# Kernel optimization log

Measured on AMD Instinct MI355X. Metric: run time of the kernel, lower is better.

Reference implementation:

```python
import jax, jax.numpy as jnp
import numpy as np

B, C, D, H, W = 16, 8, 511, 16, 16
NHEADS = 16
DIM = C * H * W          # 2048 hidden size
SEQ = D + 1              # 512 tokens incl. cls
HEAD_DIM = DIM // NHEADS # 128


def setup_inputs() -> dict:
    key = jax.random.key(0)
    ks = jax.random.split(key, 8)
    s = 0.02  # weight init scale
    return {
        "x": jax.random.normal(ks[0], (B, C, D, H, W), jnp.float32),
        "pos_embedding": jax.random.normal(ks[1], (1, SEQ, DIM), jnp.float32),
        "cls": jax.random.normal(ks[2], (1, 1, DIM), jnp.float32),
        "qkv_w": jax.random.normal(ks[3], (DIM, 3 * DIM), jnp.float32) * s,
        "qkv_b": jnp.zeros((3 * DIM,), jnp.float32),
        "proj_w": jax.random.normal(ks[4], (DIM, DIM), jnp.float32) * s,
        "proj_b": jnp.zeros((DIM,), jnp.float32),
    }


def reference(x, pos_embedding, cls, qkv_w, qkv_b, proj_w, proj_b):
    b = x.shape[0]
    # rearrange 'b c d h w -> b d (c h w)'
    tok = jnp.transpose(x, (0, 2, 1, 3, 4)).reshape(b, D, DIM)
    tok = jnp.concatenate([jnp.broadcast_to(cls, (b, 1, DIM)), tok], axis=1)
    tok = tok + pos_embedding  # (b, SEQ, DIM)
    # qkv projection (dropout probs are 0 -> identity)
    qkv = tok @ qkv_w + qkv_b  # (b, SEQ, 3*DIM)
    qkv = qkv.reshape(b, SEQ, 3, NHEADS, HEAD_DIM).transpose(2, 0, 3, 1, 4)
    q, k, v = qkv[0], qkv[1], qkv[2]  # each (b, nH, SEQ, hd)
    scale = HEAD_DIM ** -0.5
    score = jax.nn.softmax(jnp.einsum('bhqd,bhkd->bhqk', q, k) * scale, axis=-1)
    out = jnp.einsum('bhqk,bhkd->bhqd', score, v)
    out = out.transpose(0, 2, 1, 3).reshape(b, SEQ, DIM)
    out = out @ proj_w + proj_b
    return out[:, 0]  # cls token, (b, DIM)
```

## Files before the change

kernel.cpp:

```cpp
#include <hip/hip_runtime.h>


#define BB   16
#define CC   8
#define DD   511
#define DIM  2048
#define SEQ  512
#define NH   16
#define HD   128
#define W3   6144
#define SCALE 0.08838834764831845f

#define Q_OFF   0
#define AO_OFF  2048
#define G_OFF   34816
#define SC_OFF  34832
#define ZERO_N  165904
#define R_OFF   165904
#define RB_OFF  198672
#define U_OFF   231440

typedef __attribute__((ext_vector_type(8))) short short8;
typedef __attribute__((ext_vector_type(4))) float floatx4;

static __device__ inline short bf_hi(float f) {
  return (short)(__float_as_uint(f) >> 16);
}
static __device__ inline float bf_hif(float f) {
  return __uint_as_float(__float_as_uint(f) & 0xffff0000u);
}

__global__ __launch_bounds__(256) void k1_q(
    const float* __restrict__ pos, const float* __restrict__ cls,
    const float* __restrict__ qkv_w, const float* __restrict__ qkv_b,
    float* __restrict__ ws) {
  int n  = blockIdx.x * 256 + threadIdx.x;
  int d0 = blockIdx.y * 32;
  float acc = (blockIdx.y == 0) ? qkv_b[n] : 0.f;
#pragma unroll 8
  for (int d = d0; d < d0 + 32; ++d) {
    float t0 = cls[d] + pos[d];
    acc += t0 * qkv_w[(size_t)d * W3 + n];
  }
  atomicAdd(&ws[Q_OFF + n], acc);
}

__global__ __launch_bounds__(128) void k2_r(
    const float* __restrict__ qkv_w, const float* __restrict__ pos,
    const float* __restrict__ cls, float* __restrict__ ws) {
  __shared__ float qs[HD];
  int h = blockIdx.y;
  int d = blockIdx.x * 128 + threadIdx.x;
  if (threadIdx.x < HD) qs[threadIdx.x] = ws[Q_OFF + h * HD + threadIdx.x];
  __syncthreads();
  const float4* w4 = reinterpret_cast<const float4*>(
      qkv_w + (size_t)d * W3 + DIM + h * HD);
  float acc = 0.f;
#pragma unroll 8
  for (int e4 = 0; e4 < 32; ++e4) {
    float4 w = w4[e4];
    acc += qs[e4*4+0]*w.x + qs[e4*4+1]*w.y + qs[e4*4+2]*w.z + qs[e4*4+3]*w.w;
  }
  float r = acc * SCALE;
  int i = h * DIM + d;
  ws[R_OFF + i] = r;
  short* rb = (short*)(ws + RB_OFF);
  rb[i] = bf_hi(r);
  rb[NH * DIM + i] = bf_hi(r - bf_hif(r));
  float g = (cls[d] + pos[d]) * r;
  for (int m = 1; m < 64; m <<= 1) g += __shfl_xor(g, m, 64);
  if ((threadIdx.x & 63) == 0) atomicAdd(&ws[G_OFF + h], g);
}

__global__ __launch_bounds__(64) void k3_scores_mfma(
    const float* __restrict__ x, const float* __restrict__ pos,
    float* __restrict__ ws) {
  int jt = blockIdx.x, b = blockIdx.y, ks = blockIdx.z;
  int l  = threadIdx.x;
  int m  = l & 15;
  int kg = l >> 4;
  int jrow = 1 + jt * 16 + m;
  int jc = jrow < SEQ ? jrow : (SEQ - 1);
  const size_t xrow = (size_t)b * CC * DD * 256 + (size_t)(jc - 1) * 256;
  const short* rh = (const short*)(ws + RB_OFF);
  const short* rl = rh + NH * DIM;
  floatx4 acc = {0.f, 0.f, 0.f, 0.f};
#pragma unroll 2
  for (int kk = ks * 16; kk < ks * 16 + 16; ++kk) {
    int d0 = kk * 32 + kg * 8;
    int c = d0 >> 8, doff = d0 & 255;
    const float4* xp = reinterpret_cast<const float4*>(
        x + xrow + (size_t)c * DD * 256 + doff);
    const float4* pp = reinterpret_cast<const float4*>(
        pos + (size_t)jc * DIM + d0);
    float4 xa = xp[0], xb = xp[1];
    float4 pa = pp[0], pb = pp[1];
    float f[8] = {xa.x + pa.x, xa.y + pa.y, xa.z + pa.z, xa.w + pa.w,
                  xb.x + pb.x, xb.y + pb.y, xb.z + pb.z, xb.w + pb.w};
    short8 ahi, alo;
#pragma unroll
    for (int i = 0; i < 8; ++i) {
      ahi[i] = bf_hi(f[i]);
      alo[i] = bf_hi(f[i] - bf_hif(f[i]));
    }
    short8 bhi = *reinterpret_cast<const short8*>(rh + m * DIM + d0);
    short8 blo = *reinterpret_cast<const short8*>(rl + m * DIM + d0);
    acc = __builtin_amdgcn_mfma_f32_16x16x32_bf16(ahi, bhi, acc, 0, 0, 0);
    acc = __builtin_amdgcn_mfma_f32_16x16x32_bf16(ahi, blo, acc, 0, 0, 0);
    acc = __builtin_amdgcn_mfma_f32_16x16x32_bf16(alo, bhi, acc, 0, 0, 0);
  }
  int h = m;
#pragma unroll
  for (int reg = 0; reg < 4; ++reg) {
    int row = kg * 4 + reg;
    int j = 1 + jt * 16 + row;
    if (j < SEQ)
      atomicAdd(&ws[SC_OFF + (size_t)(b * NH + h) * SEQ + j], acc[reg]);
  }
}

__global__ __launch_bounds__(256) void k4_softmax(float* __restrict__ ws) {
  int h = blockIdx.x, b = blockIdx.y, t = threadIdx.x;
  float* sc = ws + SC_OFF + (size_t)(b * NH + h) * SEQ;
  __shared__ float red[256];
  float s0 = (t == 0) ? ws[G_OFF + h] : sc[t];
  float s1 = sc[t + 256];
  red[t] = fmaxf(s0, s1);
  __syncthreads();
  for (int s = 128; s > 0; s >>= 1) { if (t < s) red[t] = fmaxf(red[t], red[t + s]); __syncthreads(); }
  float m = red[0];
  __syncthreads();
  float e0 = __expf(s0 - m), e1 = __expf(s1 - m);
  red[t] = e0 + e1;
  __syncthreads();
  for (int s = 128; s > 0; s >>= 1) { if (t < s) red[t] += red[t + s]; __syncthreads(); }
  float inv = 1.f / red[0];
  sc[t] = e0 * inv;
  sc[t + 256] = e1 * inv;
}

#define PSTR 520
__global__ __launch_bounds__(256) void k5_pv_mfma(
    const float* __restrict__ x, const float* __restrict__ pos,
    const float* __restrict__ cls, float* __restrict__ ws) {
  int dt = blockIdx.x, b = blockIdx.y, t = threadIdx.x;
  __shared__ short phl[NH * PSTR];
  __shared__ short pll[NH * PSTR];
  const float* pb = ws + SC_OFF + (size_t)b * NH * SEQ;
  for (int i = t; i < NH * SEQ; i += 256) {
    int h = i >> 9, j = i & 511;
    float v = pb[h * SEQ + j];
    phl[h * PSTR + j] = bf_hi(v);
    pll[h * PSTR + j] = bf_hi(v - bf_hif(v));
  }
  __syncthreads();
  int w = t >> 6, l = t & 63;
  int m16 = l & 15, kq = l >> 4;
  int dcol = dt * 64 + w * 16 + m16;
  int c = dcol >> 8, doff = dcol & 255;
  const float* xcol = x + (size_t)b * CC * DD * 256 + (size_t)c * DD * 256 + doff;
  const float* pcol = pos + dcol;
  float clsv0 = cls[dcol];
  const short8* pph = reinterpret_cast<const short8*>(&phl[m16 * PSTR]);
  const short8* ppl = reinterpret_cast<const short8*>(&pll[m16 * PSTR]);
  floatx4 acc = {0.f, 0.f, 0.f, 0.f};
  for (int kk = 0; kk < 16; ++kk) {
    int jb = kk * 32 + kq * 8;
    const float* xp = xcol + ((size_t)jb - 1) * 256;
    const float* xp_safe = (jb == 0) ? xcol : xp;
    float f[8];
    float x0 = xp_safe[0];
    f[0] = ((jb == 0) ? clsv0 : x0) + pcol[(size_t)jb * DIM];
#pragma unroll
    for (int e = 1; e < 8; ++e)
      f[e] = xp[(size_t)e * 256] + pcol[(size_t)(jb + e) * DIM];
    short8 thi, tlo;
#pragma unroll
    for (int i = 0; i < 8; ++i) {
      thi[i] = bf_hi(f[i]);
      tlo[i] = bf_hi(f[i] - bf_hif(f[i]));
    }
    short8 phi = pph[kk * 4 + kq];
    short8 plo = ppl[kk * 4 + kq];
    acc = __builtin_amdgcn_mfma_f32_16x16x32_bf16(phi, thi, acc, 0, 0, 0);
    acc = __builtin_amdgcn_mfma_f32_16x16x32_bf16(phi, tlo, acc, 0, 0, 0);
    acc = __builtin_amdgcn_mfma_f32_16x16x32_bf16(plo, thi, acc, 0, 0, 0);
  }
  float* ub = ws + U_OFF + (size_t)b * NH * DIM + dcol;
#pragma unroll
  for (int reg = 0; reg < 4; ++reg) {
    int h = kq * 4 + reg;
    ub[(size_t)h * DIM] = acc[reg];
  }
}

__global__ __launch_bounds__(256) void k6_ao(
    const float* __restrict__ qkv_w, const float* __restrict__ qkv_b,
    float* __restrict__ ws) {
  int nt = blockIdx.x, dc = blockIdx.y, t = threadIdx.x;
  int m = nt * 256 + t;
  int h0 = nt * 2;
  int d0 = dc * 32;
  __shared__ float us[2][32][20];
  for (int i = t; i < 2 * 32 * BB; i += 256) {
    int dd = i & 31, b = (i >> 5) & 15, hh = i >> 9;
    us[hh][dd][b] = ws[U_OFF + (size_t)(b * NH + h0 + hh) * DIM + d0 + dd];
  }
  __syncthreads();
  int hl = t >> 7;
  float acc[BB];
#pragma unroll
  for (int b = 0; b < BB; ++b) acc[b] = 0.f;
  const float* wcol = qkv_w + (size_t)d0 * W3 + 2 * DIM + m;
#pragma unroll 4
  for (int dd = 0; dd < 32; ++dd) {
    float w = wcol[(size_t)dd * W3];
    const float4* u4 = reinterpret_cast<const float4*>(&us[hl][dd][0]);
    float4 u0 = u4[0], u1 = u4[1], u2 = u4[2], u3 = u4[3];
    acc[0]  += u0.x * w; acc[1]  += u0.y * w; acc[2]  += u0.z * w; acc[3]  += u0.w * w;
    acc[4]  += u1.x * w; acc[5]  += u1.y * w; acc[6]  += u1.z * w; acc[7]  += u1.w * w;
    acc[8]  += u2.x * w; acc[9]  += u2.y * w; acc[10] += u2.z * w; acc[11] += u2.w * w;
    acc[12] += u3.x * w; acc[13] += u3.y * w; acc[14] += u3.z * w; acc[15] += u3.w * w;
  }
  float bias = (dc == 0) ? qkv_b[2 * DIM + m] : 0.f;
#pragma unroll
  for (int b = 0; b < BB; ++b)
    atomicAdd(&ws[AO_OFF + b * DIM + m], acc[b] + bias);
}

__global__ __launch_bounds__(256) void k7_out(
    const float* __restrict__ proj_w, const float* __restrict__ proj_b,
    const float* __restrict__ ws, float* __restrict__ out) {
  int nt = blockIdx.x, mc = blockIdx.y, t = threadIdx.x;
  int n = nt * 256 + t;
  int m0 = mc * 32;
  __shared__ float as[32][20];
  for (int i = t; i < 32 * BB; i += 256) {
    int mm = i & 31, b = i >> 5;
    as[mm][b] = ws[AO_OFF + b * DIM + m0 + mm];
  }
  __syncthreads();
  float acc[BB];
#pragma unroll
  for (int b = 0; b < BB; ++b) acc[b] = 0.f;
  const float* wcol = proj_w + (size_t)m0 * DIM + n;
#pragma unroll 4
  for (int mm = 0; mm < 32; ++mm) {
    float w = wcol[(size_t)mm * DIM];
    const float4* a4 = reinterpret_cast<const float4*>(&as[mm][0]);
    float4 a0 = a4[0], a1 = a4[1], a2 = a4[2], a3 = a4[3];
    acc[0]  += a0.x * w; acc[1]  += a0.y * w; acc[2]  += a0.z * w; acc[3]  += a0.w * w;
    acc[4]  += a1.x * w; acc[5]  += a1.y * w; acc[6]  += a1.z * w; acc[7]  += a1.w * w;
    acc[8]  += a2.x * w; acc[9]  += a2.y * w; acc[10] += a2.z * w; acc[11] += a2.w * w;
    acc[12] += a3.x * w; acc[13] += a3.y * w; acc[14] += a3.z * w; acc[15] += a3.w * w;
  }
  float bias = (mc == 0) ? proj_b[n] : 0.f;
#pragma unroll
  for (int b = 0; b < BB; ++b)
    atomicAdd(&out[b * DIM + n], acc[b] + bias);
}

extern "C" void kernel_launch(void* const* d_in, const int* in_sizes, int n_in,
                              void* d_out, int out_size, void* d_ws, size_t ws_size,
                              hipStream_t stream) {
  const float* x      = (const float*)d_in[0];
  const float* pos    = (const float*)d_in[1];
  const float* cls    = (const float*)d_in[2];
  const float* qkv_w  = (const float*)d_in[3];
  const float* qkv_b  = (const float*)d_in[4];
  const float* proj_w = (const float*)d_in[5];
  const float* proj_b = (const float*)d_in[6];
  float* ws  = (float*)d_ws;
  float* out = (float*)d_out;

  hipMemsetAsync(ws, 0, (size_t)ZERO_N * sizeof(float), stream);
  hipMemsetAsync(out, 0, (size_t)out_size * sizeof(float), stream);

  k1_q          <<<dim3(8, 64),     256, 0, stream>>>(pos, cls, qkv_w, qkv_b, ws);
  k2_r          <<<dim3(16, 16),    128, 0, stream>>>(qkv_w, pos, cls, ws);
  k3_scores_mfma<<<dim3(32, 16, 4),  64, 0, stream>>>(x, pos, ws);
  k4_softmax    <<<dim3(16, 16),    256, 0, stream>>>(ws);
  k5_pv_mfma    <<<dim3(32, 16),    256, 0, stream>>>(x, pos, cls, ws);
  k6_ao         <<<dim3(8, 64),     256, 0, stream>>>(qkv_w, qkv_b, ws);
  k7_out        <<<dim3(8, 64),     256, 0, stream>>>(proj_w, proj_b, ws, out);
}
```

Measured before the change: 222.1 us.

## Fuse all seven stages into one cooperative persistent kernel with grid syncs

```diff
diff --git a/kernel.cpp b/kernel.cpp
--- a/kernel.cpp
+++ b/kernel.cpp
@@ -1,4 +1,7 @@
 #include <hip/hip_runtime.h>
+#include <hip/hip_cooperative_groups.h>
+
+namespace cg = cooperative_groups;
 
 
 #define BB   16
@@ -10,15 +13,18 @@
 #define HD   128
 #define W3   6144
 #define SCALE 0.08838834764831845f
+#define GRID 512
 
 #define Q_OFF   0
-#define AO_OFF  2048
-#define G_OFF   34816
+#define G_OFF   2048
+#define AO_OFF  2064
 #define SC_OFF  34832
 #define ZERO_N  165904
 #define R_OFF   165904
 #define RB_OFF  198672
 #define U_OFF   231440
+
+#define PSTR 520
 
 typedef __attribute__((ext_vector_type(8))) short short8;
 typedef __attribute__((ext_vector_type(4))) float floatx4;
@@ -30,234 +36,252 @@
   return __uint_as_float(__float_as_uint(f) & 0xffff0000u);
 }
 
-__global__ __launch_bounds__(256) void k1_q(
-    const float* __restrict__ pos, const float* __restrict__ cls,
-    const float* __restrict__ qkv_w, const float* __restrict__ qkv_b,
-    float* __restrict__ ws) {
-  int n  = blockIdx.x * 256 + threadIdx.x;
-  int d0 = blockIdx.y * 32;
-  float acc = (blockIdx.y == 0) ? qkv_b[n] : 0.f;
+struct PVShared { short phl[NH * PSTR]; short pll[NH * PSTR]; };
+union Shared {
+  PVShared pv;
+  float qs[HD];
+  float red[256];
+  float us[2][32][20];
+  float as[32][20];
+};
+
+__global__ __launch_bounds__(256, 2) void vit_fused(
+    const float* __restrict__ x, const float* __restrict__ pos,
+    const float* __restrict__ cls, const float* __restrict__ qkv_w,
+    const float* __restrict__ qkv_b, const float* __restrict__ proj_w,
+    const float* __restrict__ proj_b, float* __restrict__ ws,
+    float* __restrict__ out) {
+  cg::grid_group grid = cg::this_grid();
+  __shared__ Shared sh;
+  const int blk = blockIdx.x;
+  const int t   = threadIdx.x;
+
+  for (int i = blk * 256 + t; i < ZERO_N; i += GRID * 256) ws[i] = 0.f;
+  for (int i = blk * 256 + t; i < BB * DIM; i += GRID * 256) out[i] = 0.f;
+  grid.sync();
+
+  {
+    int nt = blk & 7, dch = blk >> 3;
+    int n = nt * 256 + t, d0 = dch * 32;
+    float acc = (dch == 0) ? qkv_b[n] : 0.f;
 #pragma unroll 8
-  for (int d = d0; d < d0 + 32; ++d) {
-    float t0 = cls[d] + pos[d];
-    acc += t0 * qkv_w[(size_t)d * W3 + n];
-  }
-  atomicAdd(&ws[Q_OFF + n], acc);
-}
-
-__global__ __launch_bounds__(128) void k2_r(
-    const float* __restrict__ qkv_w, const float* __restrict__ pos,
-    const float* __restrict__ cls, float* __restrict__ ws) {
-  __shared__ float qs[HD];
-  int h = blockIdx.y;
-  int d = blockIdx.x * 128 + threadIdx.x;
-  if (threadIdx.x < HD) qs[threadIdx.x] = ws[Q_OFF + h * HD + threadIdx.x];
-  __syncthreads();
-  const float4* w4 = reinterpret_cast<const float4*>(
-      qkv_w + (size_t)d * W3 + DIM + h * HD);
-  float acc = 0.f;
+    for (int d = d0; d < d0 + 32; ++d) {
+      float t0 = cls[d] + pos[d];
+      acc += t0 * qkv_w[(size_t)d * W3 + n];
+    }
+    atomicAdd(&ws[Q_OFF + n], acc);
+  }
+  grid.sync();
+
+  if (blk < 128) {
+    int h = blk >> 3, dt = blk & 7;
+    int d = dt * 256 + t;
+    if (t < HD) sh.qs[t] = ws[Q_OFF + h * HD + t];
+    __syncthreads();
+    const float4* w4 = reinterpret_cast<const float4*>(
+        qkv_w + (size_t)d * W3 + DIM + h * HD);
+    float acc = 0.f;
 #pragma unroll 8
-  for (int e4 = 0; e4 < 32; ++e4) {
-    float4 w = w4[e4];
-    acc += qs[e4*4+0]*w.x + qs[e4*4+1]*w.y + qs[e4*4+2]*w.z + qs[e4*4+3]*w.w;
-  }
-  float r = acc * SCALE;
-  int i = h * DIM + d;
-  ws[R_OFF + i] = r;
-  short* rb = (short*)(ws + RB_OFF);
-  rb[i] = bf_hi(r);
-  rb[NH * DIM + i] = bf_hi(r - bf_hif(r));
-  float g = (cls[d] + pos[d]) * r;
-  for (int m = 1; m < 64; m <<= 1) g += __shfl_xor(g, m, 64);
-  if ((threadIdx.x & 63) == 0) atomicAdd(&ws[G_OFF + h], g);
-}
-
-__global__ __launch_bounds__(64) void k3_scores_mfma(
-    const float* __restrict__ x, const float* __restrict__ pos,
-    float* __restrict__ ws) {
-  int jt = blockIdx.x, b = blockIdx.y, ks = blockIdx.z;
-  int l  = threadIdx.x;
-  int m  = l & 15;
-  int kg = l >> 4;
-  int jrow = 1 + jt * 16 + m;
-  int jc = jrow < SEQ ? jrow : (SEQ - 1);
-  const size_t xrow = (size_t)b * CC * DD * 256 + (size_t)(jc - 1) * 256;
-  const short* rh = (const short*)(ws + RB_OFF);
-  const short* rl = rh + NH * DIM;
-  floatx4 acc = {0.f, 0.f, 0.f, 0.f};
+    for (int e4 = 0; e4 < 32; ++e4) {
+      float4 w = w4[e4];
+      acc += sh.qs[e4*4+0]*w.x + sh.qs[e4*4+1]*w.y
+           + sh.qs[e4*4+2]*w.z + sh.qs[e4*4+3]*w.w;
+    }
+    float r = acc * SCALE;
+    int i = h * DIM + d;
+    ws[R_OFF + i] = r;
+    short* rb = (short*)(ws + RB_OFF);
+    rb[i] = bf_hi(r);
+    rb[NH * DIM + i] = bf_hi(r - bf_hif(r));
+    float g = (cls[d] + pos[d]) * r;
+    for (int m = 1; m < 64; m <<= 1) g += __shfl_xor(g, m, 64);
+    if ((t & 63) == 0) atomicAdd(&ws[G_OFF + h], g);
+  }
+  grid.sync();
+
+  {
+    int jt2 = blk & 7, b = (blk >> 3) & 15, ks = blk >> 7;
+    int w = t >> 6, l = t & 63;
+    int jt = jt2 * 4 + w;
+    int m16 = l & 15, kg = l >> 4;
+    int jrow = 1 + jt * 16 + m16;
+    int jc = jrow < SEQ ? jrow : (SEQ - 1);
+    const size_t xrow = (size_t)b * CC * DD * 256 + (size_t)(jc - 1) * 256;
+    const short* rh = (const short*)(ws + RB_OFF);
+    const short* rl = rh + NH * DIM;
+    floatx4 acc = {0.f, 0.f, 0.f, 0.f};
 #pragma unroll 2
-  for (int kk = ks * 16; kk < ks * 16 + 16; ++kk) {
-    int d0 = kk * 32 + kg * 8;
-    int c = d0 >> 8, doff = d0 & 255;
-    const float4* xp = reinterpret_cast<const float4*>(
-        x + xrow + (size_t)c * DD * 256 + doff);
-    const float4* pp = reinterpret_cast<const float4*>(
-        pos + (size_t)jc * DIM + d0);
-    float4 xa = xp[0], xb = xp[1];
-    float4 pa = pp[0], pb = pp[1];
-    float f[8] = {xa.x + pa.x, xa.y + pa.y, xa.z + pa.z, xa.w + pa.w,
-                  xb.x + pb.x, xb.y + pb.y, xb.z + pb.z, xb.w + pb.w};
-    short8 ahi, alo;
-#pragma unroll
-    for (int i = 0; i < 8; ++i) {
-      ahi[i] = bf_hi(f[i]);
-      alo[i] = bf_hi(f[i] - bf_hif(f[i]));
-    }
-    short8 bhi = *reinterpret_cast<const short8*>(rh + m * DIM + d0);
-    short8 blo = *reinterpret_cast<const short8*>(rl + m * DIM + d0);
-    acc = __builtin_amdgcn_mfma_f32_16x16x32_bf16(ahi, bhi, acc, 0, 0, 0);
-    acc = __builtin_amdgcn_mfma_f32_16x16x32_bf16(ahi, blo, acc, 0, 0, 0);
-    acc = __builtin_amdgcn_mfma_f32_16x16x32_bf16(alo, bhi, acc, 0, 0, 0);
-  }
-  int h = m;
-#pragma unroll
-  for (int reg = 0; reg < 4; ++reg) {
-    int row = kg * 4 + reg;
-    int j = 1 + jt * 16 + row;
-    if (j < SEQ)
-      atomicAdd(&ws[SC_OFF + (size_t)(b * NH + h) * SEQ + j], acc[reg]);
-  }
-}
-
-__global__ __launch_bounds__(256) void k4_softmax(float* __restrict__ ws) {
-  int h = blockIdx.x, b = blockIdx.y, t = threadIdx.x;
-  float* sc = ws + SC_OFF + (size_t)(b * NH + h) * SEQ;
-  __shared__ float red[256];
-  float s0 = (t == 0) ? ws[G_OFF + h] : sc[t];
-  float s1 = sc[t + 256];
-  red[t] = fmaxf(s0, s1);
-  __syncthreads();
-  for (int s = 128; s > 0; s >>= 1) { if (t < s) red[t] = fmaxf(red[t], red[t + s]); __syncthreads(); }
-  float m = red[0];
-  __syncthreads();
-  float e0 = __expf(s0 - m), e1 = __expf(s1 - m);
-  red[t] = e0 + e1;
-  __syncthreads();
-  for (int s = 128; s > 0; s >>= 1) { if (t < s) red[t] += red[t + s]; __syncthreads(); }
-  float inv = 1.f / red[0];
-  sc[t] = e0 * inv;
-  sc[t + 256] = e1 * inv;
-}
-
-#define PSTR 520
-__global__ __launch_bounds__(256) void k5_pv_mfma(
-    const float* __restrict__ x, const float* __restrict__ pos,
-    const float* __restrict__ cls, float* __restrict__ ws) {
-  int dt = blockIdx.x, b = blockIdx.y, t = threadIdx.x;
-  __shared__ short phl[NH * PSTR];
-  __shared__ short pll[NH * PSTR];
-  const float* pb = ws + SC_OFF + (size_t)b * NH * SEQ;
-  for (int i = t; i < NH * SEQ; i += 256) {
-    int h = i >> 9, j = i & 511;
-    float v = pb[h * SEQ + j];
-    phl[h * PSTR + j] = bf_hi(v);
-    pll[h * PSTR + j] = bf_hi(v - bf_hif(v));
-  }
-  __syncthreads();
-  int w = t >> 6, l = t & 63;
-  int m16 = l & 15, kq = l >> 4;
-  int dcol = dt * 64 + w * 16 + m16;
-  int c = dcol >> 8, doff = dcol & 255;
-  const float* xcol = x + (size_t)b * CC * DD * 256 + (size_t)c * DD * 256 + doff;
-  const float* pcol = pos + dcol;
-  float clsv0 = cls[dcol];
-  const short8* pph = reinterpret_cast<const short8*>(&phl[m16 * PSTR]);
-  const short8* ppl = reinterpret_cast<const short8*>(&pll[m16 * PSTR]);
-  floatx4 acc = {0.f, 0.f, 0.f, 0.f};
-  for (int kk = 0; kk < 16; ++kk) {
-    int jb = kk * 32 + kq * 8;
-    const float* xp = xcol + ((size_t)jb - 1) * 256;
-    const float* xp_safe = (jb == 0) ? xcol : xp;
-    float f[8];
-    float x0 = xp_safe[0];
-    f[0] = ((jb == 0) ? clsv0 : x0) + pcol[(size_t)jb * DIM];
-#pragma unroll
-    for (int e = 1; e < 8; ++e)
-      f[e] = xp[(size_t)e * 256] + pcol[(size_t)(jb + e) * DIM];
-    short8 thi, tlo;
-#pragma unroll
-    for (int i = 0; i < 8; ++i) {
-      thi[i] = bf_hi(f[i]);
-      tlo[i] = bf_hi(f[i] - bf_hif(f[i]));
-    }
-    short8 phi = pph[kk * 4 + kq];
-    short8 plo = ppl[kk * 4 + kq];
-    acc = __builtin_amdgcn_mfma_f32_16x16x32_bf16(phi, thi, acc, 0, 0, 0);
-    acc = __builtin_amdgcn_mfma_f32_16x16x32_bf16(phi, tlo, acc, 0, 0, 0);
-    acc = __builtin_amdgcn_mfma_f32_16x16x32_bf16(plo, thi, acc, 0, 0, 0);
-  }
-  float* ub = ws + U_OFF + (size_t)b * NH * DIM + dcol;
-#pragma unroll
-  for (int reg = 0; reg < 4; ++reg) {
-    int h = kq * 4 + reg;
-    ub[(size_t)h * DIM] = acc[reg];
-  }
-}
-
-__global__ __launch_bounds__(256) void k6_ao(
-    const float* __restrict__ qkv_w, const float* __restrict__ qkv_b,
-    float* __restrict__ ws) {
-  int nt = blockIdx.x, dc = blockIdx.y, t = threadIdx.x;
-  int m = nt * 256 + t;
-  int h0 = nt * 2;
-  int d0 = dc * 32;
-  __shared__ float us[2][32][20];
-  for (int i = t; i < 2 * 32 * BB; i += 256) {
-    int dd = i & 31, b = (i >> 5) & 15, hh = i >> 9;
-    us[hh][dd][b] = ws[U_OFF + (size_t)(b * NH + h0 + hh) * DIM + d0 + dd];
-  }
-  __syncthreads();
-  int hl = t >> 7;
-  float acc[BB];
-#pragma unroll
-  for (int b = 0; b < BB; ++b) acc[b] = 0.f;
-  const float* wcol = qkv_w + (size_t)d0 * W3 + 2 * DIM + m;
+    for (int kk = ks * 16; kk < ks * 16 + 16; ++kk) {
+      int d0 = kk * 32 + kg * 8;
+      int c = d0 >> 8, doff = d0 & 255;
+      const float4* xp = reinterpret_cast<const float4*>(
+          x + xrow + (size_t)c * DD * 256 + doff);
+      const float4* pp = reinterpret_cast<const float4*>(
+          pos + (size_t)jc * DIM + d0);
+      float4 xa = xp[0], xb = xp[1];
+      float4 pa = pp[0], pb = pp[1];
+      float f[8] = {xa.x + pa.x, xa.y + pa.y, xa.z + pa.z, xa.w + pa.w,
+                    xb.x + pb.x, xb.y + pb.y, xb.z + pb.z, xb.w + pb.w};
+      short8 ahi, alo;
+#pragma unroll
+      for (int i = 0; i < 8; ++i) {
+        ahi[i] = bf_hi(f[i]);
+        alo[i] = bf_hi(f[i] - bf_hif(f[i]));
+      }
+      short8 bhi = *reinterpret_cast<const short8*>(rh + m16 * DIM + d0);
+      short8 blo = *reinterpret_cast<const short8*>(rl + m16 * DIM + d0);
+      acc = __builtin_amdgcn_mfma_f32_16x16x32_bf16(ahi, bhi, acc, 0, 0, 0);
+      acc = __builtin_amdgcn_mfma_f32_16x16x32_bf16(ahi, blo, acc, 0, 0, 0);
+      acc = __builtin_amdgcn_mfma_f32_16x16x32_bf16(alo, bhi, acc, 0, 0, 0);
+    }
+    int h = m16;
+#pragma unroll
+    for (int reg = 0; reg < 4; ++reg) {
+      int row = kg * 4 + reg;
+      int j = 1 + jt * 16 + row;
+      if (j < SEQ)
+        atomicAdd(&ws[SC_OFF + (size_t)(b * NH + h) * SEQ + j], acc[reg]);
+    }
+  }
+  grid.sync();
+
+  if (blk < 256) {
+    int h = blk & 15, b = blk >> 4;
+    float* sc = ws + SC_OFF + (size_t)(b * NH + h) * SEQ;
+    float s0 = (t == 0) ? ws[G_OFF + h] : sc[t];
+    float s1 = sc[t + 256];
+    sh.red[t] = fmaxf(s0, s1);
+    __syncthreads();
+    for (int s = 128; s > 0; s >>= 1) {
+      if (t < s) sh.red[t] = fmaxf(sh.red[t], sh.red[t + s]);
+      __syncthreads();
+    }
+    float m = sh.red[0];
+    __syncthreads();
+    float e0 = __expf(s0 - m), e1 = __expf(s1 - m);
+    sh.red[t] = e0 + e1;
+    __syncthreads();
+    for (int s = 128; s > 0; s >>= 1) {
+      if (t < s) sh.red[t] += sh.red[t + s];
+      __syncthreads();
+    }
+    float inv = 1.f / sh.red[0];
+    sc[t] = e0 * inv;
+    sc[t + 256] = e1 * inv;
+  }
+  grid.sync();
+
+  {
+    int dt = blk & 31, b = blk >> 5;
+    const float* pb = ws + SC_OFF + (size_t)b * NH * SEQ;
+    for (int i = t; i < NH * SEQ; i += 256) {
+      int h = i >> 9, j = i & 511;
+      float v = pb[h * SEQ + j];
+      sh.pv.phl[h * PSTR + j] = bf_hi(v);
+      sh.pv.pll[h * PSTR + j] = bf_hi(v - bf_hif(v));
+    }
+    __syncthreads();
+    int w = t >> 6, l = t & 63;
+    int m16 = l & 15, kq = l >> 4;
+    int dcol = dt * 64 + w * 16 + m16;
+    int c = dcol >> 8, doff = dcol & 255;
+    const float* xcol = x + (size_t)b * CC * DD * 256 + (size_t)c * DD * 256 + doff;
+    const float* pcol = pos + dcol;
+    float clsv0 = cls[dcol];
+    const short8* pph = reinterpret_cast<const short8*>(&sh.pv.phl[m16 * PSTR]);
+    const short8* ppl = reinterpret_cast<const short8*>(&sh.pv.pll[m16 * PSTR]);
+    floatx4 acc = {0.f, 0.f, 0.f, 0.f};
+    for (int kk = 0; kk < 16; ++kk) {
+      int jb = kk * 32 + kq * 8;
+      const float* xp = xcol + ((size_t)jb - 1) * 256;
+      const float* xp_safe = (jb == 0) ? xcol : xp;
+      float f[8];
+      float x0 = xp_safe[0];
+      f[0] = ((jb == 0) ? clsv0 : x0) + pcol[(size_t)jb * DIM];
+#pragma unroll
+      for (int e = 1; e < 8; ++e)
+        f[e] = xp[(size_t)e * 256] + pcol[(size_t)(jb + e) * DIM];
+      short8 thi, tlo;
+#pragma unroll
+      for (int i = 0; i < 8; ++i) {
+        thi[i] = bf_hi(f[i]);
+        tlo[i] = bf_hi(f[i] - bf_hif(f[i]));
+      }
+      short8 phi = pph[kk * 4 + kq];
+      short8 plo = ppl[kk * 4 + kq];
+      acc = __builtin_amdgcn_mfma_f32_16x16x32_bf16(phi, thi, acc, 0, 0, 0);
+      acc = __builtin_amdgcn_mfma_f32_16x16x32_bf16(phi, tlo, acc, 0, 0, 0);
+      acc = __builtin_amdgcn_mfma_f32_16x16x32_bf16(plo, thi, acc, 0, 0, 0);
+    }
+    float* ub = ws + U_OFF + (size_t)b * NH * DIM + dcol;
+#pragma unroll
+    for (int reg = 0; reg < 4; ++reg) {
+      int h = kq * 4 + reg;
+      ub[(size_t)h * DIM] = acc[reg];
+    }
+  }
+  grid.sync();
+
+  {
+    int nt = blk & 7, dc = blk >> 3;
+    int m = nt * 256 + t;
+    int h0 = nt * 2;
+    int d0 = dc * 32;
+    for (int i = t; i < 2 * 32 * BB; i += 256) {
+      int dd = i & 31, b = (i >> 5) & 15, hh = i >> 9;
+      sh.us[hh][dd][b] = ws[U_OFF + (size_t)(b * NH + h0 + hh) * DIM + d0 + dd];
+    }
+    __syncthreads();
+    int hl = t >> 7;
+    float acc[BB];
+#pragma unroll
+    for (int b = 0; b < BB; ++b) acc[b] = 0.f;
+    const float* wcol = qkv_w + (size_t)d0 * W3 + 2 * DIM + m;
 #pragma unroll 4
-  for (int dd = 0; dd < 32; ++dd) {
-    float w = wcol[(size_t)dd * W3];
-    const float4* u4 = reinterpret_cast<const float4*>(&us[hl][dd][0]);
-    float4 u0 = u4[0], u1 = u4[1], u2 = u4[2], u3 = u4[3];
-    acc[0]  += u0.x * w; acc[1]  += u0.y * w; acc[2]  += u0.z * w; acc[3]  += u0.w * w;
-    acc[4]  += u1.x * w; acc[5]  += u1.y * w; acc[6]  += u1.z * w; acc[7]  += u1.w * w;
-    acc[8]  += u2.x * w; acc[9]  += u2.y * w; acc[10] += u2.z * w; acc[11] += u2.w * w;
-    acc[12] += u3.x * w; acc[13] += u3.y * w; acc[14] += u3.z * w; acc[15] += u3.w * w;
-  }
-  float bias = (dc == 0) ? qkv_b[2 * DIM + m] : 0.f;
-#pragma unroll
-  for (int b = 0; b < BB; ++b)
-    atomicAdd(&ws[AO_OFF + b * DIM + m], acc[b] + bias);
-}
-
-__global__ __launch_bounds__(256) void k7_out(
-    const float* __restrict__ proj_w, const float* __restrict__ proj_b,
-    const float* __restrict__ ws, float* __restrict__ out) {
-  int nt = blockIdx.x, mc = blockIdx.y, t = threadIdx.x;
-  int n = nt * 256 + t;
-  int m0 = mc * 32;
-  __shared__ float as[32][20];
-  for (int i = t; i < 32 * BB; i += 256) {
-    int mm = i & 31, b = i >> 5;
-    as[mm][b] = ws[AO_OFF + b * DIM + m0 + mm];
-  }
-  __syncthreads();
-  float acc[BB];
-#pragma unroll
-  for (int b = 0; b < BB; ++b) acc[b] = 0.f;
-  const float* wcol = proj_w + (size_t)m0 * DIM + n;
+    for (int dd = 0; dd < 32; ++dd) {
+      float w = wcol[(size_t)dd * W3];
+      const float4* u4 = reinterpret_cast<const float4*>(&sh.us[hl][dd][0]);
+      float4 u0 = u4[0], u1 = u4[1], u2 = u4[2], u3 = u4[3];
+      acc[0]  += u0.x * w; acc[1]  += u0.y * w; acc[2]  += u0.z * w; acc[3]  += u0.w * w;
+      acc[4]  += u1.x * w; acc[5]  += u1.y * w; acc[6]  += u1.z * w; acc[7]  += u1.w * w;
+      acc[8]  += u2.x * w; acc[9]  += u2.y * w; acc[10] += u2.z * w; acc[11] += u2.w * w;
+      acc[12] += u3.x * w; acc[13] += u3.y * w; acc[14] += u3.z * w; acc[15] += u3.w * w;
+    }
+    float bias = (dc == 0) ? qkv_b[2 * DIM + m] : 0.f;
+#pragma unroll
+    for (int b = 0; b < BB; ++b)
+      atomicAdd(&ws[AO_OFF + b * DIM + m], acc[b] + bias);
+  }
+  grid.sync();
+
+  {
+    int nt = blk & 7, mc = blk >> 3;
+    int n = nt * 256 + t;
+    int m0 = mc * 32;
+    for (int i = t; i < 32 * BB; i += 256) {
+      int mm = i & 31, b = i >> 5;
+      sh.as[mm][b] = ws[AO_OFF + b * DIM + m0 + mm];
+    }
+    __syncthreads();
+    float acc[BB];
+#pragma unroll
+    for (int b = 0; b < BB; ++b) acc[b] = 0.f;
+    const float* wcol = proj_w + (size_t)m0 * DIM + n;
 #pragma unroll 4
-  for (int mm = 0; mm < 32; ++mm) {
-    float w = wcol[(size_t)mm * DIM];
-    const float4* a4 = reinterpret_cast<const float4*>(&as[mm][0]);
-    float4 a0 = a4[0], a1 = a4[1], a2 = a4[2], a3 = a4[3];
-    acc[0]  += a0.x * w; acc[1]  += a0.y * w; acc[2]  += a0.z * w; acc[3]  += a0.w * w;
-    acc[4]  += a1.x * w; acc[5]  += a1.y * w; acc[6]  += a1.z * w; acc[7]  += a1.w * w;
-    acc[8]  += a2.x * w; acc[9]  += a2.y * w; acc[10] += a2.z * w; acc[11] += a2.w * w;
-    acc[12] += a3.x * w; acc[13] += a3.y * w; acc[14] += a3.z * w; acc[15] += a3.w * w;
-  }
-  float bias = (mc == 0) ? proj_b[n] : 0.f;
-#pragma unroll
-  for (int b = 0; b < BB; ++b)
-    atomicAdd(&out[b * DIM + n], acc[b] + bias);
+    for (int mm = 0; mm < 32; ++mm) {
+      float w = wcol[(size_t)mm * DIM];
+      const float4* a4 = reinterpret_cast<const float4*>(&sh.as[mm][0]);
+      float4 a0 = a4[0], a1 = a4[1], a2 = a4[2], a3 = a4[3];
+      acc[0]  += a0.x * w; acc[1]  += a0.y * w; acc[2]  += a0.z * w; acc[3]  += a0.w * w;
+      acc[4]  += a1.x * w; acc[5]  += a1.y * w; acc[6]  += a1.z * w; acc[7]  += a1.w * w;
+      acc[8]  += a2.x * w; acc[9]  += a2.y * w; acc[10] += a2.z * w; acc[11] += a2.w * w;
+      acc[12] += a3.x * w; acc[13] += a3.y * w; acc[14] += a3.z * w; acc[15] += a3.w * w;
+    }
+    float bias = (mc == 0) ? proj_b[n] : 0.f;
+#pragma unroll
+    for (int b = 0; b < BB; ++b)
+      atomicAdd(&out[b * DIM + n], acc[b] + bias);
+  }
 }
 
 extern "C" void kernel_launch(void* const* d_in, const int* in_sizes, int n_in,
@@ -273,14 +297,9 @@
   float* ws  = (float*)d_ws;
   float* out = (float*)d_out;
 
-  hipMemsetAsync(ws, 0, (size_t)ZERO_N * sizeof(float), stream);
-  hipMemsetAsync(out, 0, (size_t)out_size * sizeof(float), stream);
-
-  k1_q          <<<dim3(8, 64),     256, 0, stream>>>(pos, cls, qkv_w, qkv_b, ws);
-  k2_r          <<<dim3(16, 16),    128, 0, stream>>>(qkv_w, pos, cls, ws);
-  k3_scores_mfma<<<dim3(32, 16, 4),  64, 0, stream>>>(x, pos, ws);
-  k4_softmax    <<<dim3(16, 16),    256, 0, stream>>>(ws);
-  k5_pv_mfma    <<<dim3(32, 16),    256, 0, stream>>>(x, pos, cls, ws);
-  k6_ao         <<<dim3(8, 64),     256, 0, stream>>>(qkv_w, qkv_b, ws);
-  k7_out        <<<dim3(8, 64),     256, 0, stream>>>(proj_w, proj_b, ws, out);
+  void* kargs[] = {(void*)&x, (void*)&pos, (void*)&cls, (void*)&qkv_w,
+                   (void*)&qkv_b, (void*)&proj_w, (void*)&proj_b,
+                   (void*)&ws, (void*)&out};
+  hipLaunchCooperativeKernel((void*)vit_fused, dim3(GRID), dim3(256),
+                             kargs, 0, stream);
 }
```

After: 617.1 us. 178% more time.

## Fuse softmax into PV kernel, replace memsets with prep kernel, transpose pos

Applied to the files above, without the earlier changes.

```diff
diff --git a/kernel.cpp b/kernel.cpp
--- a/kernel.cpp
+++ b/kernel.cpp
@@ -12,13 +12,16 @@
 #define SCALE 0.08838834764831845f
 
 #define Q_OFF   0
-#define AO_OFF  2048
-#define G_OFF   34816
+#define G_OFF   2048
+#define AO_OFF  2064
 #define SC_OFF  34832
 #define ZERO_N  165904
 #define R_OFF   165904
 #define RB_OFF  198672
 #define U_OFF   231440
+#define POST_OFF 755728
+
+#define PSTR 520
 
 typedef __attribute__((ext_vector_type(8))) short short8;
 typedef __attribute__((ext_vector_type(4))) float floatx4;
@@ -28,6 +31,26 @@
 }
 static __device__ inline float bf_hif(float f) {
   return __uint_as_float(__float_as_uint(f) & 0xffff0000u);
+}
+
+__global__ __launch_bounds__(256) void k0_prep(
+    const float* __restrict__ pos, float* __restrict__ ws,
+    float* __restrict__ out) {
+  int blk = blockIdx.x + blockIdx.y * 16;
+  int t = threadIdx.x;
+  for (int i = blk * 256 + t; i < ZERO_N; i += 1024 * 256) ws[i] = 0.f;
+  for (int i = blk * 256 + t; i < BB * DIM; i += 1024 * 256) out[i] = 0.f;
+  __shared__ float tile[32][33];
+  int jt = blockIdx.x, dt = blockIdx.y;
+  int tx = t & 31, ty = t >> 5;
+#pragma unroll
+  for (int r = 0; r < 32; r += 8)
+    tile[ty + r][tx] = pos[(size_t)(jt * 32 + ty + r) * DIM + dt * 32 + tx];
+  __syncthreads();
+  float* pt = ws + POST_OFF;
+#pragma unroll
+  for (int r = 0; r < 32; r += 8)
+    pt[(size_t)(dt * 32 + ty + r) * SEQ + jt * 32 + tx] = tile[tx][ty + r];
 }
 
 __global__ __launch_bounds__(256) void k1_q(
@@ -72,14 +95,15 @@
   if ((threadIdx.x & 63) == 0) atomicAdd(&ws[G_OFF + h], g);
 }
 
-__global__ __launch_bounds__(64) void k3_scores_mfma(
+__global__ __launch_bounds__(256) void k3_scores_mfma(
     const float* __restrict__ x, const float* __restrict__ pos,
     float* __restrict__ ws) {
-  int jt = blockIdx.x, b = blockIdx.y, ks = blockIdx.z;
-  int l  = threadIdx.x;
-  int m  = l & 15;
-  int kg = l >> 4;
-  int jrow = 1 + jt * 16 + m;
+  int jt2 = blockIdx.x, b = blockIdx.y, ks = blockIdx.z;
+  int t = threadIdx.x;
+  int w = t >> 6, l = t & 63;
+  int jt = jt2 * 4 + w;
+  int m16 = l & 15, kg = l >> 4;
+  int jrow = 1 + jt * 16 + m16;
   int jc = jrow < SEQ ? jrow : (SEQ - 1);
   const size_t xrow = (size_t)b * CC * DD * 256 + (size_t)(jc - 1) * 256;
   const short* rh = (const short*)(ws + RB_OFF);
@@ -103,13 +127,13 @@
       ahi[i] = bf_hi(f[i]);
       alo[i] = bf_hi(f[i] - bf_hif(f[i]));
     }
-    short8 bhi = *reinterpret_cast<const short8*>(rh + m * DIM + d0);
-    short8 blo = *reinterpret_cast<const short8*>(rl + m * DIM + d0);
+    short8 bhi = *reinterpret_cast<const short8*>(rh + m16 * DIM + d0);
+    short8 blo = *reinterpret_cast<const short8*>(rl + m16 * DIM + d0);
     acc = __builtin_amdgcn_mfma_f32_16x16x32_bf16(ahi, bhi, acc, 0, 0, 0);
     acc = __builtin_amdgcn_mfma_f32_16x16x32_bf16(ahi, blo, acc, 0, 0, 0);
     acc = __builtin_amdgcn_mfma_f32_16x16x32_bf16(alo, bhi, acc, 0, 0, 0);
   }
-  int h = m;
+  int h = m16;
 #pragma unroll
   for (int reg = 0; reg < 4; ++reg) {
     int row = kg * 4 + reg;
@@ -119,47 +143,44 @@
   }
 }
 
-__global__ __launch_bounds__(256) void k4_softmax(float* __restrict__ ws) {
-  int h = blockIdx.x, b = blockIdx.y, t = threadIdx.x;
-  float* sc = ws + SC_OFF + (size_t)(b * NH + h) * SEQ;
-  __shared__ float red[256];
-  float s0 = (t == 0) ? ws[G_OFF + h] : sc[t];
-  float s1 = sc[t + 256];
-  red[t] = fmaxf(s0, s1);
-  __syncthreads();
-  for (int s = 128; s > 0; s >>= 1) { if (t < s) red[t] = fmaxf(red[t], red[t + s]); __syncthreads(); }
-  float m = red[0];
-  __syncthreads();
-  float e0 = __expf(s0 - m), e1 = __expf(s1 - m);
-  red[t] = e0 + e1;
-  __syncthreads();
-  for (int s = 128; s > 0; s >>= 1) { if (t < s) red[t] += red[t + s]; __syncthreads(); }
-  float inv = 1.f / red[0];
-  sc[t] = e0 * inv;
-  sc[t + 256] = e1 * inv;
-}
-
-#define PSTR 520
 __global__ __launch_bounds__(256) void k5_pv_mfma(
-    const float* __restrict__ x, const float* __restrict__ pos,
-    const float* __restrict__ cls, float* __restrict__ ws) {
+    const float* __restrict__ x, const float* __restrict__ cls,
+    float* __restrict__ ws) {
   int dt = blockIdx.x, b = blockIdx.y, t = threadIdx.x;
   __shared__ short phl[NH * PSTR];
   __shared__ short pll[NH * PSTR];
-  const float* pb = ws + SC_OFF + (size_t)b * NH * SEQ;
-  for (int i = t; i < NH * SEQ; i += 256) {
-    int h = i >> 9, j = i & 511;
-    float v = pb[h * SEQ + j];
-    phl[h * PSTR + j] = bf_hi(v);
-    pll[h * PSTR + j] = bf_hi(v - bf_hif(v));
-  }
-  __syncthreads();
   int w = t >> 6, l = t & 63;
+  for (int rr = 0; rr < 4; ++rr) {
+    int h = w * 4 + rr;
+    const float* sch = ws + SC_OFF + (size_t)(b * NH + h) * SEQ;
+    float gam = ws[G_OFF + h];
+    float s[8];
+#pragma unroll
+    for (int i = 0; i < 8; ++i) s[i] = sch[i * 64 + l];
+    if (l == 0) s[0] = gam;
+    float mx = s[0];
+#pragma unroll
+    for (int i = 1; i < 8; ++i) mx = fmaxf(mx, s[i]);
+    for (int m = 1; m < 64; m <<= 1) mx = fmaxf(mx, __shfl_xor(mx, m, 64));
+    float e[8], sum = 0.f;
+#pragma unroll
+    for (int i = 0; i < 8; ++i) { e[i] = __expf(s[i] - mx); sum += e[i]; }
+    for (int m = 1; m < 64; m <<= 1) sum += __shfl_xor(sum, m, 64);
+    float inv = 1.f / sum;
+#pragma unroll
+    for (int i = 0; i < 8; ++i) {
+      float p = e[i] * inv;
+      int j = i * 64 + l;
+      phl[h * PSTR + j] = bf_hi(p);
+      pll[h * PSTR + j] = bf_hi(p - bf_hif(p));
+    }
+  }
+  __syncthreads();
   int m16 = l & 15, kq = l >> 4;
   int dcol = dt * 64 + w * 16 + m16;
   int c = dcol >> 8, doff = dcol & 255;
   const float* xcol = x + (size_t)b * CC * DD * 256 + (size_t)c * DD * 256 + doff;
-  const float* pcol = pos + dcol;
+  const float* ptcol = ws + POST_OFF + (size_t)dcol * SEQ;
   float clsv0 = cls[dcol];
   const short8* pph = reinterpret_cast<const short8*>(&phl[m16 * PSTR]);
   const short8* ppl = reinterpret_cast<const short8*>(&pll[m16 * PSTR]);
@@ -168,12 +189,15 @@
     int jb = kk * 32 + kq * 8;
     const float* xp = xcol + ((size_t)jb - 1) * 256;
     const float* xp_safe = (jb == 0) ? xcol : xp;
+    const float4* pt4 = reinterpret_cast<const float4*>(ptcol + jb);
+    float4 pt0 = pt4[0], pt1 = pt4[1];
+    float ptv[8] = {pt0.x, pt0.y, pt0.z, pt0.w, pt1.x, pt1.y, pt1.z, pt1.w};
     float f[8];
     float x0 = xp_safe[0];
-    f[0] = ((jb == 0) ? clsv0 : x0) + pcol[(size_t)jb * DIM];
+    f[0] = ((jb == 0) ? clsv0 : x0) + ptv[0];
 #pragma unroll
     for (int e = 1; e < 8; ++e)
-      f[e] = xp[(size_t)e * 256] + pcol[(size_t)(jb + e) * DIM];
+      f[e] = xp[(size_t)e * 256] + ptv[e];
     short8 thi, tlo;
 #pragma unroll
     for (int i = 0; i < 8; ++i) {
@@ -273,14 +297,11 @@
   float* ws  = (float*)d_ws;
   float* out = (float*)d_out;
 
-  hipMemsetAsync(ws, 0, (size_t)ZERO_N * sizeof(float), stream);
-  hipMemsetAsync(out, 0, (size_t)out_size * sizeof(float), stream);
-
+  k0_prep       <<<dim3(16, 64),    256, 0, stream>>>(pos, ws, out);
   k1_q          <<<dim3(8, 64),     256, 0, stream>>>(pos, cls, qkv_w, qkv_b, ws);
   k2_r          <<<dim3(16, 16),    128, 0, stream>>>(qkv_w, pos, cls, ws);
-  k3_scores_mfma<<<dim3(32, 16, 4),  64, 0, stream>>>(x, pos, ws);
-  k4_softmax    <<<dim3(16, 16),    256, 0, stream>>>(ws);
-  k5_pv_mfma    <<<dim3(32, 16),    256, 0, stream>>>(x, pos, cls, ws);
+  k3_scores_mfma<<<dim3(8, 16, 4),  256, 0, stream>>>(x, pos, ws);
+  k5_pv_mfma    <<<dim3(32, 16),    256, 0, stream>>>(x, cls, ws);
   k6_ao         <<<dim3(8, 64),     256, 0, stream>>>(qkv_w, qkv_b, ws);
   k7_out        <<<dim3(8, 64),     256, 0, stream>>>(proj_w, proj_b, ws, out);
 }
```

After: 220.1 us. About the same (-0.9%).
